# Kernel tuning notes

Measured on AMD Instinct MI355X. Metric: run time of the kernel, lower is better.

The kernel has to match this reference:

```python
import jax, jax.numpy as jnp
import numpy as np
import math

D_MODEL = 256
N_LEVELS = 4
N_HEADS = 8
N_POINTS = 4
SPATIAL = [[92, 160], [46, 80], [23, 40], [12, 20]]  # (H_l, W_l)
BATCH = 8
LEN_Q = 8192


def setup_inputs() -> dict:
    key = jax.random.key(0)
    ks = jax.random.split(key, 8)
    len_in = sum(h * w for h, w in SPATIAL)
    query = jax.random.normal(ks[0], (BATCH, LEN_Q, D_MODEL), jnp.float32)
    reference_points = jax.random.uniform(ks[1], (BATCH, LEN_Q, N_LEVELS, 2), jnp.float32)
    input_flatten = jax.random.normal(ks[2], (BATCH, len_in, D_MODEL), jnp.float32)
    input_spatial_shapes = jnp.array(SPATIAL, jnp.int32)
    starts = np.cumsum([0] + [h * w for h, w in SPATIAL])[:-1]
    input_level_start_index = jnp.array(starts, jnp.int32)
    # learned params (sampling_offsets bias uses the directional grid init from _reset_parameters)
    W_off = jax.random.normal(ks[3], (D_MODEL, N_HEADS * N_LEVELS * N_POINTS * 2), jnp.float32) * 0.01
    thetas = jnp.arange(N_HEADS, dtype=jnp.float32) * (2.0 * math.pi / N_HEADS)
    grid = jnp.stack([jnp.cos(thetas), jnp.sin(thetas)], -1)
    grid = grid / jnp.max(jnp.abs(grid), axis=-1, keepdims=True)
    grid = jnp.tile(grid[:, None, None, :], (1, N_LEVELS, N_POINTS, 1))
    grid = grid * jnp.arange(1, N_POINTS + 1, dtype=jnp.float32)[None, None, :, None]
    b_off = grid.reshape(-1)
    W_attn = jax.random.normal(ks[4], (D_MODEL, N_HEADS * N_LEVELS * N_POINTS), jnp.float32) * 0.02
    b_attn = jnp.zeros((N_HEADS * N_LEVELS * N_POINTS,), jnp.float32)
    W_val = jax.random.normal(ks[5], (D_MODEL, D_MODEL), jnp.float32) * (1.0 / math.sqrt(D_MODEL))
    b_val = jnp.zeros((D_MODEL,), jnp.float32)
    W_out = jax.random.normal(ks[6], (D_MODEL, D_MODEL), jnp.float32) * (1.0 / math.sqrt(D_MODEL))
    b_out = jnp.zeros((D_MODEL,), jnp.float32)
    return dict(query=query, reference_points=reference_points, input_flatten=input_flatten,
                input_spatial_shapes=input_spatial_shapes,
                input_level_start_index=input_level_start_index,
                W_off=W_off, b_off=b_off, W_attn=W_attn, b_attn=b_attn,
                W_val=W_val, b_val=b_val, W_out=W_out, b_out=b_out)


def _ms_deform_attn(query, reference_points, input_flatten, spatial_shapes_np,
                    W_off, b_off, W_attn, b_attn, W_val, b_val, W_out, b_out):
    Nb, Lq, C = query.shape
    Hh, L, P = N_HEADS, N_LEVELS, N_POINTS
    Dh = C // Hh
    value = (input_flatten @ W_val + b_val).reshape(Nb, -1, Hh, Dh)
    attn = (query @ W_attn + b_attn).reshape(Nb, Lq, Hh, L * P)
    attn = jax.nn.softmax(attn, axis=-1).reshape(Nb, Lq, Hh, L, P)
    off = (query @ W_off + b_off).reshape(Nb, Lq, Hh, L, P, 2)
    # offset_normalizer = (W_l, H_l)
    norm = jnp.asarray(np.stack([spatial_shapes_np[:, 1], spatial_shapes_np[:, 0]], -1),
                       dtype=query.dtype)  # (L, 2)
    loc = reference_points[:, :, None, :, None, :] + off / norm[None, None, None, :, None, :]
    out = jnp.zeros((Nb, Lq, Hh, Dh), query.dtype)
    start = 0
    for l in range(L):
        H, W = int(spatial_shapes_np[l, 0]), int(spatial_shapes_np[l, 1])
        v = value[:, start:start + H * W]                       # (Nb, H*W, Hh, Dh)
        start += H * W
        v = v.transpose(0, 2, 1, 3).reshape(Nb * Hh, H * W, Dh)  # (B2, H*W, Dh)
        g = loc[:, :, :, l].transpose(0, 2, 1, 3, 4).reshape(Nb * Hh, Lq * P, 2)
        # grid_sample with grid = 2*loc-1, align_corners=False, zero padding
        x = g[..., 0] * W - 0.5
        y = g[..., 1] * H - 0.5
        x0f = jnp.floor(x); y0f = jnp.floor(y)
        wx = x - x0f; wy = y - y0f
        x0 = x0f.astype(jnp.int32); y0 = y0f.astype(jnp.int32)

        def gather(xi, yi):
            valid = (xi >= 0) & (xi < W) & (yi >= 0) & (yi < H)
            idx = jnp.clip(yi, 0, H - 1) * W + jnp.clip(xi, 0, W - 1)
            samp = jnp.take_along_axis(v, idx[..., None], axis=1)  # (B2, Lq*P, Dh)
            return samp * valid[..., None].astype(v.dtype)

        s = (gather(x0, y0) * ((1 - wx) * (1 - wy))[..., None]
             + gather(x0 + 1, y0) * (wx * (1 - wy))[..., None]
             + gather(x0, y0 + 1) * ((1 - wx) * wy)[..., None]
             + gather(x0 + 1, y0 + 1) * (wx * wy)[..., None])
        s = s.reshape(Nb, Hh, Lq, P, Dh)
        w = attn[:, :, :, l].transpose(0, 2, 1, 3)  # (Nb, Hh, Lq, P)
        out = out + jnp.einsum('bhqp,bhqpd->bqhd', w, s)
    return out.reshape(Nb, Lq, C) @ W_out + b_out


def reference(query, reference_points, input_flatten, input_spatial_shapes,
              input_level_start_index, W_off, b_off, W_attn, b_attn,
              W_val, b_val, W_out, b_out):
    # spatial shapes are static metadata (define per-level view sizes)
    shapes_np = np.asarray(input_spatial_shapes)
    del input_level_start_index  # levels are contiguous; starts derived from shapes
    return _ms_deform_attn(query, reference_points, input_flatten, shapes_np,
                           W_off, b_off, W_attn, b_attn, W_val, b_val, W_out, b_out)
```

## Files before the change

### kernel.cpp

```cpp
#include <hip/hip_runtime.h>
#include <hip/hip_bf16.h>
#include <cstddef>
#include <cstdint>

#define NB 8
#define LQ 8192
#define DMODEL 256
#define NHD 8
#define NLV 4
#define NPT 4
#define LEN_IN 19560
#define NQ (NB * LQ)
#define MV (NB * LEN_IN)
#define MVP 156544

using bf16x8 = __attribute__((ext_vector_type(8))) short;
using f32x4  = __attribute__((ext_vector_type(4))) float;

typedef const __attribute__((address_space(1))) void* gas_ptr;
typedef __attribute__((address_space(3))) void* las_ptr;

__device__ __forceinline__ void gl_lds16(const void* g, void* l) {
  __builtin_amdgcn_global_load_lds((gas_ptr)g, (las_ptr)l, 16, 0, 0);
}
__device__ __forceinline__ float bflo(unsigned u) {
  union { unsigned i; float f; } c; c.i = u << 16; return c.f;
}
__device__ __forceinline__ float bfhi(unsigned u) {
  union { unsigned i; float f; } c; c.i = u & 0xffff0000u; return c.f;
}
__device__ __forceinline__ bf16x8 pack8(float4 a, float4 b) {
  bf16x8 o;
  o[0] = (short)__bfloat16_as_ushort(__float2bfloat16(a.x));
  o[1] = (short)__bfloat16_as_ushort(__float2bfloat16(a.y));
  o[2] = (short)__bfloat16_as_ushort(__float2bfloat16(a.z));
  o[3] = (short)__bfloat16_as_ushort(__float2bfloat16(a.w));
  o[4] = (short)__bfloat16_as_ushort(__float2bfloat16(b.x));
  o[5] = (short)__bfloat16_as_ushort(__float2bfloat16(b.y));
  o[6] = (short)__bfloat16_as_ushort(__float2bfloat16(b.z));
  o[7] = (short)__bfloat16_as_ushort(__float2bfloat16(b.w));
  return o;
}

__global__ __launch_bounds__(256) void transpose_bf16(
    const float* __restrict__ W, __hip_bfloat16* __restrict__ Bt, int N) {
  const int o = blockIdx.x * 256 + threadIdx.x;
  const int n = o >> 8, k = o & 255;
  Bt[o] = __float2bfloat16(W[(size_t)k * N + n]);
}

template <int OUT_MODE, int A_F32, int NT>
__global__ __launch_bounds__(512) void gemm_mfma(
    const void* __restrict__ Av, const __hip_bfloat16* __restrict__ Bt,
    const float* __restrict__ bias, const float* __restrict__ bias2,
    void* __restrict__ Cout, void* __restrict__ Cout2, int M_valid) {
  constexpr int NJ = NT / 64;
  __shared__ __hip_bfloat16 As[128 * 32];
  __shared__ __hip_bfloat16 Bs[NT * 32];

  const int tid = threadIdx.x;
  const int wv = tid >> 6;
  const int lane = tid & 63;
  const int quad = lane >> 4;
  const int l16 = lane & 15;
  const int bm = blockIdx.x * 128;
  const int rw = (wv & 1) * 64;
  const int cwave = (wv >> 1) * (NT / 4);

  const __hip_bfloat16* gB = Bt + (size_t)(tid >> 2) * 256 + (tid & 3) * 8;

  const __hip_bfloat16* gA16 = nullptr;
  const float* gA32 = nullptr;
  __hip_bfloat16* dA = nullptr;
  bool okA = true;
  if (A_F32) {
    const int r = tid >> 2, seg = tid & 3;
    okA = (bm + r) < M_valid;
    gA32 = (const float*)Av + (size_t)(bm + r) * 256 + seg * 8;
    dA = As + r * 32 + seg * 8;
  } else {
    gA16 = (const __hip_bfloat16*)Av + (size_t)(bm + (tid >> 2)) * 256 +
           (tid & 3) * 8;
  }

  f32x4 acc[4][NJ] = {};

#pragma unroll 1
  for (int k0 = 0; k0 < 256; k0 += 32) {
    float4 f0, f1;
    if (A_F32) {
      if (okA) {
        f0 = *(const float4*)(gA32 + k0);
        f1 = *(const float4*)(gA32 + k0 + 4);
      } else {
        f0 = f1 = make_float4(0.f, 0.f, 0.f, 0.f);
      }
    }
    __syncthreads();
#pragma unroll
    for (int c = 0; c < NT / 128; ++c)
      gl_lds16(gB + (size_t)c * 128 * 256 + k0,
               (char*)Bs + c * 8192 + wv * 1024);
    if (A_F32) {
      *(bf16x8*)dA = pack8(f0, f1);
    } else {
      gl_lds16(gA16 + k0, (char*)As + wv * 1024);
    }
    __syncthreads();

    bf16x8 af[4], bfr[NJ];
#pragma unroll
    for (int t = 0; t < 4; ++t)
      af[t] = *(const bf16x8*)(As + (rw + t * 16 + l16) * 32 + quad * 8);
#pragma unroll
    for (int j = 0; j < NJ; ++j)
      bfr[j] = *(const bf16x8*)(Bs + (cwave + j * 16 + l16) * 32 + quad * 8);
#pragma unroll
    for (int i = 0; i < 4; ++i)
#pragma unroll
      for (int j = 0; j < NJ; ++j)
        acc[i][j] = __builtin_amdgcn_mfma_f32_16x16x32_bf16(af[i], bfr[j],
                                                            acc[i][j], 0, 0, 0);
  }

#pragma unroll
  for (int j = 0; j < NJ; ++j) {
    const int col = cwave + j * 16 + l16;
    float bb;
    if (OUT_MODE == 3)
      bb = (col < 128) ? bias[col] : bias2[col - 128];
    else
      bb = bias[col];
#pragma unroll
    for (int i = 0; i < 4; ++i) {
#pragma unroll
      for (int r = 0; r < 4; ++r) {
        const int row = bm + rw + i * 16 + quad * 4 + r;
        const float v = acc[i][j][r] + bb;
        if (OUT_MODE == 0) {
          ((float*)Cout)[(size_t)row * NT + col] = v;
        } else if (OUT_MODE == 2) {
          if (row < M_valid) {
            const int b = row / LEN_IN;
            const int pix = row - b * LEN_IN;
            const int h = col >> 5, ch = col & 31;
            ((__hip_bfloat16*)Cout)[(((size_t)(b * 8 + h) * LEN_IN + pix) << 5) +
                                    ch] = __float2bfloat16(v);
          }
        } else {
          if (col < 128) {
            ((float*)Cout)[(size_t)row * 128 + col] = v;
          } else {
            ((__hip_bfloat16*)Cout2)[(size_t)row * 256 + (col - 128)] =
                __float2bfloat16(v);
          }
        }
      }
    }
  }
}

__global__ __launch_bounds__(256, 4) void msda_sample6(
    const float* __restrict__ refp,
    const float* __restrict__ logits,
    const __hip_bfloat16* __restrict__ offb,
    const __hip_bfloat16* __restrict__ vh,
    __hip_bfloat16* __restrict__ mid) {
  const int q0 = blockIdx.x * 2;
  const int tid = threadIdx.x;

  __shared__ int2 s_d[2][8][17][4];

  {
    const int sq = tid >> 7;
    const int t = tid & 127;
    const int qg = q0 + sq;
    const int l = (t >> 2) & 3;
    constexpr int Hs[4] = {92, 46, 23, 12};
    constexpr int Ws_[4] = {160, 80, 40, 20};
    constexpr int St[4] = {0, 14720, 18400, 19320};
    const int Hl = Hs[l], Wl = Ws_[l];

    const float lg = logits[(size_t)qg * 128 + t];
    float mx = lg;
#pragma unroll
    for (int d = 1; d < 16; d <<= 1) mx = fmaxf(mx, __shfl_xor(mx, d));
    const float e = expf(lg - mx);
    float sm = e;
#pragma unroll
    for (int d = 1; d < 16; d <<= 1) sm += __shfl_xor(sm, d);
    const float w = e / sm;

    const float rx = refp[(size_t)qg * 8 + 2 * l];
    const float ry = refp[(size_t)qg * 8 + 2 * l + 1];
    const unsigned uo = *(const unsigned*)(offb + (size_t)qg * 256 + 2 * t);
    const float ox = bflo(uo), oy = bfhi(uo);

    const float x = rx * (float)Wl + ox - 0.5f;
    const float y = ry * (float)Hl + oy - 0.5f;
    const float xf = floorf(x), yf = floorf(y);
    const float wx = x - xf, wy = y - yf;
    const int x0 = (int)xf, y0 = (int)yf;
    const int x1 = x0 + 1, y1 = y0 + 1;
    const bool vx0 = (x0 >= 0) & (x0 < Wl), vx1 = (x1 >= 0) & (x1 < Wl);
    const bool vy0 = (y0 >= 0) & (y0 < Hl), vy1 = (y1 >= 0) & (y1 < Hl);
    const int cx0 = min(max(x0, 0), Wl - 1), cx1 = min(max(x1, 0), Wl - 1);
    const int cy0 = min(max(y0, 0), Hl - 1), cy1 = min(max(y1, 0), Hl - 1);

    const int o00 = (St[l] + cy0 * Wl + cx0) * 64;
    const int o01 = (St[l] + cy1 * Wl + cx0) * 64;
    const int dx = (cx1 - cx0) * 64;

    int2* dd = s_d[sq][t >> 4][t & 15];
    dd[0] = make_int2(o00,      __float_as_int((vx0 & vy0) ? w * (1.f - wx) * (1.f - wy) : 0.f));
    dd[1] = make_int2(o00 + dx, __float_as_int((vx1 & vy0) ? w * wx * (1.f - wy) : 0.f));
    dd[2] = make_int2(o01,      __float_as_int((vx0 & vy1) ? w * (1.f - wx) * wy : 0.f));
    dd[3] = make_int2(o01 + dx, __float_as_int((vx1 & vy1) ? w * wx * wy : 0.f));
  }
  __syncthreads();

  const int tap = tid & 3;
  const int cg = (tid >> 2) & 3;
  const int h = (tid >> 4) & 7;
  const int sq = tid >> 7;
  const int qg = q0 + sq;
  const int bq = q0 >> 13;

  const char* vbase = (const char*)vh + (size_t)bq * (8ULL * LEN_IN * 64);
  const int voff0 = h * (LEN_IN * 64) + cg * 16;
  const int2* sd = &s_d[sq][h][0][tap];

  float w[16];
  uint4 u[16];
#pragma unroll
  for (int j = 0; j < 16; ++j) {
    const int2 dw = sd[j * 4];
    w[j] = __int_as_float(dw.y);
    u[j] = *(const uint4*)(vbase + (unsigned)(voff0 + dw.x));
  }

  float a[8] = {};
#pragma unroll
  for (int j = 0; j < 16; ++j) {
    a[0] += w[j] * bflo(u[j].x); a[1] += w[j] * bfhi(u[j].x);
    a[2] += w[j] * bflo(u[j].y); a[3] += w[j] * bfhi(u[j].y);
    a[4] += w[j] * bflo(u[j].z); a[5] += w[j] * bfhi(u[j].z);
    a[6] += w[j] * bflo(u[j].w); a[7] += w[j] * bfhi(u[j].w);
  }

#pragma unroll
  for (int i = 0; i < 8; ++i) a[i] += __shfl_xor(a[i], 1);
#pragma unroll
  for (int i = 0; i < 8; ++i) a[i] += __shfl_xor(a[i], 2);

  if (tap == 0) {
    unsigned short* mp =
        (unsigned short*)mid + (size_t)qg * 256 + h * 32 + cg * 8;
    int4 o;
    o.x = (int)((unsigned)__bfloat16_as_ushort(__float2bfloat16(a[0])) |
                ((unsigned)__bfloat16_as_ushort(__float2bfloat16(a[1])) << 16));
    o.y = (int)((unsigned)__bfloat16_as_ushort(__float2bfloat16(a[2])) |
                ((unsigned)__bfloat16_as_ushort(__float2bfloat16(a[3])) << 16));
    o.z = (int)((unsigned)__bfloat16_as_ushort(__float2bfloat16(a[4])) |
                ((unsigned)__bfloat16_as_ushort(__float2bfloat16(a[5])) << 16));
    o.w = (int)((unsigned)__bfloat16_as_ushort(__float2bfloat16(a[6])) |
                ((unsigned)__bfloat16_as_ushort(__float2bfloat16(a[7])) << 16));
    *(int4*)mp = o;
  }
}

extern "C" void kernel_launch(void* const* d_in, const int* in_sizes, int n_in,
                              void* d_out, int out_size, void* d_ws,
                              size_t ws_size, hipStream_t stream) {
  const float* query = (const float*)d_in[0];
  const float* refp = (const float*)d_in[1];
  const float* inflat = (const float*)d_in[2];
  const float* W_off = (const float*)d_in[5];
  const float* b_off = (const float*)d_in[6];
  const float* W_attn = (const float*)d_in[7];
  const float* b_attn = (const float*)d_in[8];
  const float* W_val = (const float*)d_in[9];
  const float* b_val = (const float*)d_in[10];
  const float* W_out = (const float*)d_in[11];
  const float* b_out = (const float*)d_in[12];
  float* out = (float*)d_out;

  char* ws = (char*)d_ws;
  __hip_bfloat16* vh = (__hip_bfloat16*)(ws);
  float* logits = (float*)(ws + 80117760ULL);
  __hip_bfloat16* offb = (__hip_bfloat16*)(ws + 113672192ULL);
  __hip_bfloat16* mid = (__hip_bfloat16*)(ws + 147226624ULL);
  __hip_bfloat16* Btv = (__hip_bfloat16*)(ws + 180781056ULL);
  __hip_bfloat16* Btc = (__hip_bfloat16*)(ws + 180912128ULL);
  __hip_bfloat16* Btw = (__hip_bfloat16*)(ws + 181108736ULL);

  transpose_bf16<<<256, 256, 0, stream>>>(W_val, Btv, 256);
  transpose_bf16<<<128, 256, 0, stream>>>(W_attn, Btc, 128);
  transpose_bf16<<<256, 256, 0, stream>>>(W_off, Btc + 128 * 256, 256);
  transpose_bf16<<<256, 256, 0, stream>>>(W_out, Btw, 256);

  gemm_mfma<2, 1, 256><<<MVP / 128, 512, 0, stream>>>(
      inflat, Btv, b_val, nullptr, vh, nullptr, MV);
  gemm_mfma<3, 1, 384><<<NQ / 128, 512, 0, stream>>>(
      query, Btc, b_attn, b_off, logits, offb, NQ);
  msda_sample6<<<NQ / 2, 256, 0, stream>>>(refp, logits, offb, vh, mid);
  gemm_mfma<0, 0, 256><<<NQ / 128, 512, 0, stream>>>(
      mid, Btw, b_out, nullptr, out, nullptr, NQ);
}
```

Before: 530.1 us.

## Keep full B matrix resident in LDS with persistent GEMM blocks; asm loads in sampler

Replaces the K-tiled GEMM with a persistent kernel that loads the whole transposed weight matrix into XOR-swizzled LDS once per block. A operands are read straight from global memory into registers through a three-deep software pipeline, and the block loops over 64-row chunks. The goal is to remove repeated B reloads, per-K-step barriers and the A staging through LDS. The sampling kernel now issues its gathers as inline-asm global loads with a single waitcnt, and its occupancy hint drops from 4 to 3 blocks. The large LDS footprint and higher register use limit occupancy, and the fixed grid of 256 blocks may underfill the device.

```diff
diff --git a/kernel.cpp b/kernel.cpp
--- a/kernel.cpp
+++ b/kernel.cpp
@@ -12,10 +12,10 @@
 #define LEN_IN 19560
 #define NQ (NB * LQ)
 #define MV (NB * LEN_IN)
-#define MVP 156544
 
 using bf16x8 = __attribute__((ext_vector_type(8))) short;
 using f32x4  = __attribute__((ext_vector_type(4))) float;
+using u32x4  = __attribute__((ext_vector_type(4))) unsigned int;
 
 typedef const __attribute__((address_space(1))) void* gas_ptr;
 typedef __attribute__((address_space(3))) void* las_ptr;
@@ -50,117 +50,143 @@
 }
 
 template <int OUT_MODE, int A_F32, int NT>
-__global__ __launch_bounds__(512) void gemm_mfma(
+__global__ __launch_bounds__(256) void gemm_bres(
     const void* __restrict__ Av, const __hip_bfloat16* __restrict__ Bt,
     const float* __restrict__ bias, const float* __restrict__ bias2,
-    void* __restrict__ Cout, void* __restrict__ Cout2, int M_valid) {
+    void* __restrict__ Cout, void* __restrict__ Cout2, int nchunks) {
   constexpr int NJ = NT / 64;
-  __shared__ __hip_bfloat16 As[128 * 32];
-  __shared__ __hip_bfloat16 Bs[NT * 32];
+  __shared__ __hip_bfloat16 Bs[NT * 256];
 
   const int tid = threadIdx.x;
   const int wv = tid >> 6;
   const int lane = tid & 63;
   const int quad = lane >> 4;
   const int l16 = lane & 15;
-  const int bm = blockIdx.x * 128;
-  const int rw = (wv & 1) * 64;
-  const int cwave = (wv >> 1) * (NT / 4);
-
-  const __hip_bfloat16* gB = Bt + (size_t)(tid >> 2) * 256 + (tid & 3) * 8;
-
-  const __hip_bfloat16* gA16 = nullptr;
-  const float* gA32 = nullptr;
-  __hip_bfloat16* dA = nullptr;
-  bool okA = true;
-  if (A_F32) {
-    const int r = tid >> 2, seg = tid & 3;
-    okA = (bm + r) < M_valid;
-    gA32 = (const float*)Av + (size_t)(bm + r) * 256 + seg * 8;
-    dA = As + r * 32 + seg * 8;
-  } else {
-    gA16 = (const __hip_bfloat16*)Av + (size_t)(bm + (tid >> 2)) * 256 +
-           (tid & 3) * 8;
-  }
-
-  f32x4 acc[4][NJ] = {};
+  const int colbase = (OUT_MODE == 3) ? blockIdx.y * NT : 0;
+  const __hip_bfloat16* BtBlk = Bt + (size_t)colbase * 256;
+
+  for (int c = 0; c < NT / 8; ++c) {
+    const int slot = c * 4096 + tid * 16;
+    const int row = slot >> 9;
+    const int col = slot & 511;
+    const int src = (slot & ~511) | (col ^ ((row & 7) << 4));
+    gl_lds16((const char*)BtBlk + src, (char*)Bs + c * 4096 + wv * 1024);
+  }
+  __syncthreads();
+
+  const int cwave = wv * (NT / 4);
+  const int bxor = (l16 & 7) << 4;
+  const char* BsB = (const char*)Bs;
+
+#define STEP(s, AF)                                                         \
+  {                                                                         \
+    bf16x8 af_[4], bf_[NJ];                                                 \
+    _Pragma("unroll") for (int i = 0; i < 4; ++i) af_[i] = AF(i);           \
+    _Pragma("unroll") for (int j = 0; j < NJ; ++j)                          \
+      bf_[j] = *(const bf16x8*)(BsB + (cwave + j * 16 + l16) * 512 +        \
+                                ((((s) << 6) + (quad << 4)) ^ bxor));       \
+    _Pragma("unroll") for (int i = 0; i < 4; ++i)                           \
+      _Pragma("unroll") for (int j = 0; j < NJ; ++j)                        \
+        acc[i][j] = __builtin_amdgcn_mfma_f32_16x16x32_bf16(                \
+            af_[i], bf_[j], acc[i][j], 0, 0, 0);                            \
+  }
 
 #pragma unroll 1
-  for (int k0 = 0; k0 < 256; k0 += 32) {
-    float4 f0, f1;
+  for (int ch = blockIdx.x; ch < nchunks; ch += gridDim.x) {
+    f32x4 acc[4][NJ] = {};
+
     if (A_F32) {
-      if (okA) {
-        f0 = *(const float4*)(gA32 + k0);
-        f1 = *(const float4*)(gA32 + k0 + 4);
-      } else {
-        f0 = f1 = make_float4(0.f, 0.f, 0.f, 0.f);
-      }
+      const float* gA =
+          (const float*)Av + ((size_t)ch * 64 + l16) * 256 + quad * 8;
+      float4 fa0[4][2], fa1[4][2], fa2[4][2];
+#define LDA32(dst, s)                                                       \
+  _Pragma("unroll") for (int i = 0; i < 4; ++i) {                           \
+    dst[i][0] = *(const float4*)(gA + (size_t)i * 16 * 256 + (s) * 32);     \
+    dst[i][1] = *(const float4*)(gA + (size_t)i * 16 * 256 + (s) * 32 + 4); \
+  }
+#define AF0(i) pack8(fa0[i][0], fa0[i][1])
+#define AF1(i) pack8(fa1[i][0], fa1[i][1])
+#define AF2(i) pack8(fa2[i][0], fa2[i][1])
+      LDA32(fa0, 0);
+      LDA32(fa1, 1);
+      LDA32(fa2, 2);
+      STEP(0, AF0); LDA32(fa0, 3);
+      STEP(1, AF1); LDA32(fa1, 4);
+      STEP(2, AF2); LDA32(fa2, 5);
+      STEP(3, AF0); LDA32(fa0, 6);
+      STEP(4, AF1); LDA32(fa1, 7);
+      STEP(5, AF2);
+      STEP(6, AF0);
+      STEP(7, AF1);
+#undef LDA32
+#undef AF0
+#undef AF1
+#undef AF2
+    } else {
+      const __hip_bfloat16* gA =
+          (const __hip_bfloat16*)Av + ((size_t)ch * 64 + l16) * 256 + quad * 8;
+      bf16x8 ba0[4], ba1[4], ba2[4];
+#define LDA16(dst, s)                                                       \
+  _Pragma("unroll") for (int i = 0; i < 4; ++i) dst[i] =                    \
+      *(const bf16x8*)(gA + (size_t)i * 16 * 256 + (s) * 32);
+#define AFB0(i) ba0[i]
+#define AFB1(i) ba1[i]
+#define AFB2(i) ba2[i]
+      LDA16(ba0, 0);
+      LDA16(ba1, 1);
+      LDA16(ba2, 2);
+      STEP(0, AFB0); LDA16(ba0, 3);
+      STEP(1, AFB1); LDA16(ba1, 4);
+      STEP(2, AFB2); LDA16(ba2, 5);
+      STEP(3, AFB0); LDA16(ba0, 6);
+      STEP(4, AFB1); LDA16(ba1, 7);
+      STEP(5, AFB2);
+      STEP(6, AFB0);
+      STEP(7, AFB1);
+#undef LDA16
+#undef AFB0
+#undef AFB1
+#undef AFB2
     }
-    __syncthreads();
-#pragma unroll
-    for (int c = 0; c < NT / 128; ++c)
-      gl_lds16(gB + (size_t)c * 128 * 256 + k0,
-               (char*)Bs + c * 8192 + wv * 1024);
-    if (A_F32) {
-      *(bf16x8*)dA = pack8(f0, f1);
-    } else {
-      gl_lds16(gA16 + k0, (char*)As + wv * 1024);
-    }
-    __syncthreads();
-
-    bf16x8 af[4], bfr[NJ];
-#pragma unroll
-    for (int t = 0; t < 4; ++t)
-      af[t] = *(const bf16x8*)(As + (rw + t * 16 + l16) * 32 + quad * 8);
-#pragma unroll
-    for (int j = 0; j < NJ; ++j)
-      bfr[j] = *(const bf16x8*)(Bs + (cwave + j * 16 + l16) * 32 + quad * 8);
-#pragma unroll
-    for (int i = 0; i < 4; ++i)
-#pragma unroll
-      for (int j = 0; j < NJ; ++j)
-        acc[i][j] = __builtin_amdgcn_mfma_f32_16x16x32_bf16(af[i], bfr[j],
-                                                            acc[i][j], 0, 0, 0);
-  }
-
-#pragma unroll
-  for (int j = 0; j < NJ; ++j) {
-    const int col = cwave + j * 16 + l16;
-    float bb;
-    if (OUT_MODE == 3)
-      bb = (col < 128) ? bias[col] : bias2[col - 128];
-    else
-      bb = bias[col];
-#pragma unroll
-    for (int i = 0; i < 4; ++i) {
-#pragma unroll
-      for (int r = 0; r < 4; ++r) {
-        const int row = bm + rw + i * 16 + quad * 4 + r;
-        const float v = acc[i][j][r] + bb;
-        if (OUT_MODE == 0) {
-          ((float*)Cout)[(size_t)row * NT + col] = v;
-        } else if (OUT_MODE == 2) {
-          if (row < M_valid) {
+
+#pragma unroll
+    for (int j = 0; j < NJ; ++j) {
+      const int col = colbase + cwave + j * 16 + l16;
+      float bb;
+      if (OUT_MODE == 3)
+        bb = (col < 128) ? bias[col] : bias2[col - 128];
+      else
+        bb = bias[col];
+#pragma unroll
+      for (int i = 0; i < 4; ++i) {
+#pragma unroll
+        for (int r = 0; r < 4; ++r) {
+          const int row = ch * 64 + i * 16 + quad * 4 + r;
+          const float v = acc[i][j][r] + bb;
+          if (OUT_MODE == 0) {
+            ((float*)Cout)[(size_t)row * 256 + col] = v;
+          } else if (OUT_MODE == 2) {
             const int b = row / LEN_IN;
             const int pix = row - b * LEN_IN;
-            const int h = col >> 5, ch = col & 31;
+            const int h = col >> 5, chn = col & 31;
             ((__hip_bfloat16*)Cout)[(((size_t)(b * 8 + h) * LEN_IN + pix) << 5) +
-                                    ch] = __float2bfloat16(v);
-          }
-        } else {
-          if (col < 128) {
-            ((float*)Cout)[(size_t)row * 128 + col] = v;
+                                    chn] = __float2bfloat16(v);
           } else {
-            ((__hip_bfloat16*)Cout2)[(size_t)row * 256 + (col - 128)] =
-                __float2bfloat16(v);
+            if (col < 128) {
+              ((float*)Cout)[(size_t)row * 128 + col] = v;
+            } else {
+              ((__hip_bfloat16*)Cout2)[(size_t)row * 256 + (col - 128)] =
+                  __float2bfloat16(v);
+            }
           }
         }
       }
     }
   }
-}
-
-__global__ __launch_bounds__(256, 4) void msda_sample6(
+#undef STEP
+}
+
+__global__ __launch_bounds__(256, 3) void msda_sample7(
     const float* __restrict__ refp,
     const float* __restrict__ logits,
     const __hip_bfloat16* __restrict__ offb,
@@ -231,21 +257,26 @@
   const int2* sd = &s_d[sq][h][0][tap];
 
   float w[16];
-  uint4 u[16];
+  u32x4 u[16];
 #pragma unroll
   for (int j = 0; j < 16; ++j) {
     const int2 dw = sd[j * 4];
     w[j] = __int_as_float(dw.y);
-    u[j] = *(const uint4*)(vbase + (unsigned)(voff0 + dw.x));
-  }
+    const unsigned voff = (unsigned)(voff0 + dw.x);
+    asm volatile("global_load_dwordx4 %0, %1, %2"
+                 : "=v"(u[j])
+                 : "v"(voff), "s"(vbase));
+  }
+  asm volatile("s_waitcnt vmcnt(0)" ::: "memory");
+  __builtin_amdgcn_sched_barrier(0);
 
   float a[8] = {};
 #pragma unroll
   for (int j = 0; j < 16; ++j) {
-    a[0] += w[j] * bflo(u[j].x); a[1] += w[j] * bfhi(u[j].x);
-    a[2] += w[j] * bflo(u[j].y); a[3] += w[j] * bfhi(u[j].y);
-    a[4] += w[j] * bflo(u[j].z); a[5] += w[j] * bfhi(u[j].z);
-    a[6] += w[j] * bflo(u[j].w); a[7] += w[j] * bfhi(u[j].w);
+    a[0] += w[j] * bflo(u[j][0]); a[1] += w[j] * bfhi(u[j][0]);
+    a[2] += w[j] * bflo(u[j][1]); a[3] += w[j] * bfhi(u[j][1]);
+    a[4] += w[j] * bflo(u[j][2]); a[5] += w[j] * bfhi(u[j][2]);
+    a[6] += w[j] * bflo(u[j][3]); a[7] += w[j] * bfhi(u[j][3]);
   }
 
 #pragma unroll
@@ -299,11 +330,11 @@
   transpose_bf16<<<256, 256, 0, stream>>>(W_off, Btc + 128 * 256, 256);
   transpose_bf16<<<256, 256, 0, stream>>>(W_out, Btw, 256);
 
-  gemm_mfma<2, 1, 256><<<MVP / 128, 512, 0, stream>>>(
-      inflat, Btv, b_val, nullptr, vh, nullptr, MV);
-  gemm_mfma<3, 1, 384><<<NQ / 128, 512, 0, stream>>>(
-      query, Btc, b_attn, b_off, logits, offb, NQ);
-  msda_sample6<<<NQ / 2, 256, 0, stream>>>(refp, logits, offb, vh, mid);
-  gemm_mfma<0, 0, 256><<<NQ / 128, 512, 0, stream>>>(
-      mid, Btw, b_out, nullptr, out, nullptr, NQ);
-}
+  gemm_bres<2, 1, 256><<<256, 256, 0, stream>>>(
+      inflat, Btv, b_val, nullptr, vh, nullptr, MV / 64);
+  gemm_bres<3, 1, 192><<<dim3(128, 2), 256, 0, stream>>>(
+      query, Btc, b_attn, b_off, logits, offb, NQ / 64);
+  msda_sample7<<<NQ / 2, 256, 0, stream>>>(refp, logits, offb, vh, mid);
+  gemm_bres<0, 0, 256><<<256, 256, 0, stream>>>(
+      mid, Btw, b_out, nullptr, out, nullptr, NQ / 64);
+}
```

Measured after the change: 640.5 us. 1.21x slower.

## Double-buffer GEMM LDS tiles with vmcnt-based waits and XOR swizzle

Applied to the files above, without the earlier changes.

Rewrites the three projection GEMMs to use two LDS buffers, so the global-to-LDS loads for k-step t+2 are issued while k-step t computes. Waits use explicit s_waitcnt vmcnt counts in place of a pair of __syncthreads per step. An XOR swizzle of the 16-byte segments is applied to cut LDS bank conflicts on the fragment reads. This doubles LDS use and relies on hand-tuned vmcnt values that must match the number of loads in flight.

```diff
diff --git a/kernel.cpp b/kernel.cpp
--- a/kernel.cpp
+++ b/kernel.cpp
@@ -50,13 +50,14 @@
 }
 
 template <int OUT_MODE, int A_F32, int NT>
-__global__ __launch_bounds__(512) void gemm_mfma(
+__global__ __launch_bounds__(512) void gemm_cnt(
     const void* __restrict__ Av, const __hip_bfloat16* __restrict__ Bt,
     const float* __restrict__ bias, const float* __restrict__ bias2,
     void* __restrict__ Cout, void* __restrict__ Cout2, int M_valid) {
   constexpr int NJ = NT / 64;
-  __shared__ __hip_bfloat16 As[128 * 32];
-  __shared__ __hip_bfloat16 Bs[NT * 32];
+  constexpr int NCB = NT / 128;
+  __shared__ __hip_bfloat16 Asb[2][128 * 32];
+  __shared__ __hip_bfloat16 Bsb[2][NT * 32];
 
   const int tid = threadIdx.x;
   const int wv = tid >> 6;
@@ -66,62 +67,112 @@
   const int bm = blockIdx.x * 128;
   const int rw = (wv & 1) * 64;
   const int cwave = (wv >> 1) * (NT / 4);
-
-  const __hip_bfloat16* gB = Bt + (size_t)(tid >> 2) * 256 + (tid & 3) * 8;
-
-  const __hip_bfloat16* gA16 = nullptr;
+  const int swz = (tid & 3) ^ ((tid >> 3) & 3);
+  const int rsw = (quad ^ ((l16 >> 1) & 3)) << 4;
+
+  const char* gB = (const char*)Bt + (size_t)(tid >> 2) * 512 + swz * 16;
+
+  const char* gA16 = nullptr;
   const float* gA32 = nullptr;
-  __hip_bfloat16* dA = nullptr;
   bool okA = true;
   if (A_F32) {
-    const int r = tid >> 2, seg = tid & 3;
+    const int r = tid >> 2;
     okA = (bm + r) < M_valid;
-    gA32 = (const float*)Av + (size_t)(bm + r) * 256 + seg * 8;
-    dA = As + r * 32 + seg * 8;
+    gA32 = (const float*)Av + (size_t)(bm + r) * 256 + swz * 8;
   } else {
-    gA16 = (const __hip_bfloat16*)Av + (size_t)(bm + (tid >> 2)) * 256 +
-           (tid & 3) * 8;
+    gA16 = (const char*)Av + (size_t)(bm + (tid >> 2)) * 512 + swz * 16;
+  }
+  char* const dA0 = (char*)&Asb[0][0] + (tid >> 2) * 64 + (tid & 3) * 16;
+
+#define STAGE_B(t, p)                                                   \
+  { _Pragma("unroll") for (int c = 0; c < NCB; ++c)                     \
+      gl_lds16(gB + (size_t)c * 65536 + (t) * 64,                       \
+               (char*)&Bsb[p][0] + c * 8192 + wv * 1024); }
+#define STAGE_A16(t, p)                                                 \
+  gl_lds16(gA16 + (t) * 64, (char*)&Asb[p][0] + wv * 1024)
+#define LOAD_A32(t, fa)                                                 \
+  {                                                                     \
+    if (okA) {                                                          \
+      fa[0] = *(const float4*)(gA32 + (t) * 32);                        \
+      fa[1] = *(const float4*)(gA32 + (t) * 32 + 4);                    \
+    } else {                                                            \
+      fa[0] = fa[1] = make_float4(0.f, 0.f, 0.f, 0.f);                  \
+    }                                                                   \
+  }
+#define PACK_A(p, fa) *(bf16x8*)(dA0 + (p) * 8192) = pack8(fa[0], fa[1])
+#define WAIT_ISS()                                                      \
+  {                                                                     \
+    if constexpr (A_F32 && NT == 256)                                   \
+      asm volatile("s_waitcnt vmcnt(4)" ::: "memory");                  \
+    else if constexpr (A_F32 && NT == 384)                              \
+      asm volatile("s_waitcnt vmcnt(5)" ::: "memory");                  \
+    else                                                                \
+      asm volatile("s_waitcnt vmcnt(3)" ::: "memory");                  \
+    asm volatile("s_waitcnt lgkmcnt(0)" ::: "memory");                  \
+  }
+#define BAR()                                                           \
+  {                                                                     \
+    __builtin_amdgcn_sched_barrier(0);                                  \
+    __builtin_amdgcn_s_barrier();                                       \
+    __builtin_amdgcn_sched_barrier(0);                                  \
+  }
+#define COMPUTE(p)                                                      \
+  {                                                                     \
+    bf16x8 af[4], bf[NJ];                                               \
+    _Pragma("unroll") for (int i = 0; i < 4; ++i)                       \
+        af[i] = *(const bf16x8*)((const char*)&Asb[p][0] +              \
+                                 (rw + i * 16 + l16) * 64 + rsw);       \
+    _Pragma("unroll") for (int j = 0; j < NJ; ++j)                      \
+        bf[j] = *(const bf16x8*)((const char*)&Bsb[p][0] +              \
+                                 (cwave + j * 16 + l16) * 64 + rsw);    \
+    _Pragma("unroll") for (int i = 0; i < 4; ++i)                       \
+        _Pragma("unroll") for (int j = 0; j < NJ; ++j) acc[i][j] =      \
+        __builtin_amdgcn_mfma_f32_16x16x32_bf16(af[i], bf[j],           \
+                                                acc[i][j], 0, 0, 0);    \
   }
 
   f32x4 acc[4][NJ] = {};
-
-#pragma unroll 1
-  for (int k0 = 0; k0 < 256; k0 += 32) {
-    float4 f0, f1;
+  float4 faA[2], faB[2];
+
+  if (A_F32) LOAD_A32(0, faA);
+  STAGE_B(0, 0);
+  if (!A_F32) STAGE_A16(0, 0);
+  if (A_F32) LOAD_A32(1, faB);
+  STAGE_B(1, 1);
+  if (!A_F32) STAGE_A16(1, 1);
+  if (A_F32) PACK_A(0, faA);
+
+#pragma unroll
+  for (int t = 0; t < 6; ++t) {
+    WAIT_ISS();
+    BAR();
+    COMPUTE(t & 1);
+    BAR();
     if (A_F32) {
-      if (okA) {
-        f0 = *(const float4*)(gA32 + k0);
-        f1 = *(const float4*)(gA32 + k0 + 4);
-      } else {
-        f0 = f1 = make_float4(0.f, 0.f, 0.f, 0.f);
-      }
+      if ((t + 1) & 1) { PACK_A(1, faB); } else { PACK_A(0, faA); }
+      if (t & 1) { LOAD_A32(t + 2, faB); } else { LOAD_A32(t + 2, faA); }
+    } else {
+      STAGE_A16(t + 2, t & 1);
     }
-    __syncthreads();
-#pragma unroll
-    for (int c = 0; c < NT / 128; ++c)
-      gl_lds16(gB + (size_t)c * 128 * 256 + k0,
-               (char*)Bs + c * 8192 + wv * 1024);
-    if (A_F32) {
-      *(bf16x8*)dA = pack8(f0, f1);
-    } else {
-      gl_lds16(gA16 + k0, (char*)As + wv * 1024);
-    }
-    __syncthreads();
-
-    bf16x8 af[4], bfr[NJ];
-#pragma unroll
-    for (int t = 0; t < 4; ++t)
-      af[t] = *(const bf16x8*)(As + (rw + t * 16 + l16) * 32 + quad * 8);
-#pragma unroll
-    for (int j = 0; j < NJ; ++j)
-      bfr[j] = *(const bf16x8*)(Bs + (cwave + j * 16 + l16) * 32 + quad * 8);
-#pragma unroll
-    for (int i = 0; i < 4; ++i)
-#pragma unroll
-      for (int j = 0; j < NJ; ++j)
-        acc[i][j] = __builtin_amdgcn_mfma_f32_16x16x32_bf16(af[i], bfr[j],
-                                                            acc[i][j], 0, 0, 0);
-  }
+    STAGE_B(t + 2, t & 1);
+  }
+  WAIT_ISS();
+  BAR();
+  COMPUTE(0);
+  BAR();
+  if (A_F32) PACK_A(1, faB);
+  asm volatile("s_waitcnt vmcnt(0)" ::: "memory");
+  asm volatile("s_waitcnt lgkmcnt(0)" ::: "memory");
+  BAR();
+  COMPUTE(1);
+
+#undef STAGE_B
+#undef STAGE_A16
+#undef LOAD_A32
+#undef PACK_A
+#undef WAIT_ISS
+#undef BAR
+#undef COMPUTE
 
 #pragma unroll
   for (int j = 0; j < NJ; ++j) {
@@ -143,9 +194,9 @@
           if (row < M_valid) {
             const int b = row / LEN_IN;
             const int pix = row - b * LEN_IN;
-            const int h = col >> 5, ch = col & 31;
+            const int h = col >> 5, chn = col & 31;
             ((__hip_bfloat16*)Cout)[(((size_t)(b * 8 + h) * LEN_IN + pix) << 5) +
-                                    ch] = __float2bfloat16(v);
+                                    chn] = __float2bfloat16(v);
           }
         } else {
           if (col < 128) {
@@ -299,11 +350,11 @@
   transpose_bf16<<<256, 256, 0, stream>>>(W_off, Btc + 128 * 256, 256);
   transpose_bf16<<<256, 256, 0, stream>>>(W_out, Btw, 256);
 
-  gemm_mfma<2, 1, 256><<<MVP / 128, 512, 0, stream>>>(
+  gemm_cnt<2, 1, 256><<<MVP / 128, 512, 0, stream>>>(
       inflat, Btv, b_val, nullptr, vh, nullptr, MV);
-  gemm_mfma<3, 1, 384><<<NQ / 128, 512, 0, stream>>>(
+  gemm_cnt<3, 1, 384><<<NQ / 128, 512, 0, stream>>>(
       query, Btc, b_attn, b_off, logits, offb, NQ);
   msda_sample6<<<NQ / 2, 256, 0, stream>>>(refp, logits, offb, vh, mid);
-  gemm_mfma<0, 0, 256><<<NQ / 128, 512, 0, stream>>>(
+  gemm_cnt<0, 0, 256><<<NQ / 128, 512, 0, stream>>>(
       mid, Btw, b_out, nullptr, out, nullptr, NQ);
 }
```

After: 549.4 us. +3.6%, slower.
